# Kernel tuning notes

Hardware: AMD Instinct MI355X
Metric: run time of the kernel (lower is better)

## Reference

```python
import jax, jax.numpy as jnp
import numpy as np

B, S, HID = 2, 2048, 2048
NH, NKV, HD = 16, 4, 128
EPS = 1e-6
THETA = 10000.0
NEG = jnp.float32(-1e30)


def setup_inputs() -> dict:
    key = jax.random.key(0)
    ks = jax.random.split(key, 7)
    return {
        "hidden_states": jax.random.normal(ks[0], (B, S, HID), jnp.float32) * 0.02,
        "positions": jnp.broadcast_to(jnp.arange(S, dtype=jnp.int32), (B, S)),
        "Wq": jax.random.normal(ks[1], (HID, NH * HD), jnp.float32) * (HID ** -0.5),
        "Wk": jax.random.normal(ks[2], (HID, NKV * HD), jnp.float32) * (HID ** -0.5),
        "Wv": jax.random.normal(ks[3], (HID, NKV * HD), jnp.float32) * (HID ** -0.5),
        "Wc": jax.random.normal(ks[4], (NH * HD, HID), jnp.float32) * ((NH * HD) ** -0.5),
        "q_scale": jax.random.uniform(ks[5], (HD,), jnp.float32),
        "k_scale": jax.random.uniform(ks[6], (HD,), jnp.float32),
    }


def _rmsnorm(x, scale):
    # per-head RMSNorm over head_dim (nnx.RMSNorm semantics)
    return x * jax.lax.rsqrt(jnp.mean(x * x, axis=-1, keepdims=True) + EPS) * scale


def _rope_neox(x, positions):
    # x: [B, S, H, HD]; full rotary_dim == HD, neox style (split halves)
    half = HD // 2
    inv_freq = 1.0 / (THETA ** (jnp.arange(half, dtype=jnp.float32) / half))
    ang = positions[..., None].astype(jnp.float32) * inv_freq  # [B, S, half]
    cos = jnp.cos(ang)[:, :, None, :]
    sin = jnp.sin(ang)[:, :, None, :]
    x1, x2 = jnp.split(x, 2, axis=-1)
    return jnp.concatenate([x1 * cos - x2 * sin, x2 * cos + x1 * sin], axis=-1)


def reference(hidden_states, positions, Wq, Wk, Wv, Wc, q_scale, k_scale):
    q = (hidden_states @ Wq).reshape(B, S, NH, HD)
    k = (hidden_states @ Wk).reshape(B, S, NKV, HD)
    v = (hidden_states @ Wv).reshape(B, S, NKV, HD)
    q = _rmsnorm(q, q_scale)
    k = _rmsnorm(k, k_scale)
    q = _rope_neox(q, positions)
    k = _rope_neox(k, positions)
    # GQA: expand KV heads to query heads
    rep = NH // NKV
    k = jnp.repeat(k, rep, axis=2)
    v = jnp.repeat(v, rep, axis=2)
    scores = jnp.einsum("bqhd,bkhd->bhqk", q, k) * (HD ** -0.5)
    causal = jnp.tril(jnp.ones((S, S), dtype=bool))
    scores = jnp.where(causal, scores, NEG)
    probs = jax.nn.softmax(scores, axis=-1)
    attn = jnp.einsum("bhqk,bkhd->bqhd", probs, v).reshape(B, S, NH * HD)
    return attn @ Wc
```

## Files before the change

kernel.cpp:

```cpp
#include <hip/hip_runtime.h>
#include <stdint.h>

typedef unsigned short u16;
typedef unsigned int u32;
typedef __bf16 bf16x8 __attribute__((ext_vector_type(8)));
typedef float f32x4 __attribute__((ext_vector_type(4)));
typedef u32 u32x4 __attribute__((ext_vector_type(4)));

__device__ __forceinline__ u16 f2bf(float x){
  u32 u = __float_as_uint(x);
  u += 0x7FFFu + ((u >> 16) & 1u);
  return (u16)(u >> 16);
}
__device__ __forceinline__ float bf2f(u16 h){
  return __uint_as_float(((u32)h) << 16);
}
__device__ __forceinline__ u32 cvt_pk_bf16(float lo, float hi){
  u32 r;
  asm("v_cvt_pk_bf16_f32 %0, %1, %2" : "=v"(r) : "v"(lo), "v"(hi));
  return r;
}
__device__ __forceinline__ f32x4 mfma16(bf16x8 a, bf16x8 b, f32x4 c){
  return __builtin_amdgcn_mfma_f32_16x16x32_bf16(a, b, c, 0, 0, 0);
}
__device__ __forceinline__ void gload16(const void* g, const void* l){
  __builtin_amdgcn_global_load_lds(
      (__attribute__((address_space(1))) void*)(uintptr_t)g,
      (__attribute__((address_space(3))) void*)(u32)(uintptr_t)l,
      16, 0, 0);
}

__global__ void k_rope_table(float* __restrict__ ct, float* __restrict__ st){
  int idx = blockIdx.x * 256 + threadIdx.x;
  int p = idx >> 6, i = idx & 63;
  float freq = powf(10000.0f, -(float)i / 64.0f);
  float ang = (float)p * freq;
  ct[idx] = cosf(ang);
  st[idx] = sinf(ang);
}

__global__ void k_cast_bf16(const float* __restrict__ in, u16* __restrict__ out){
  int i = (blockIdx.x * 256 + threadIdx.x) * 4;
  float4 v = *(const float4*)(in + i);
  ushort4 o;
  o.x = f2bf(v.x); o.y = f2bf(v.y); o.z = f2bf(v.z); o.w = f2bf(v.w);
  *(ushort4*)(out + i) = o;
}

__global__ void k_trans_qkv(const float* __restrict__ Wq, const float* __restrict__ Wk,
                            const float* __restrict__ Wv, u16* __restrict__ out){
  __shared__ float tile[32][33];
  int nb = blockIdx.x * 32, kb = blockIdx.y * 32;
  int tx = threadIdx.x, ty = threadIdx.y;
  #pragma unroll
  for (int j = 0; j < 4; j++){
    int k = kb + ty + j*8;
    int n = nb + tx;
    float v;
    if (n < 2048)      v = Wq[(size_t)k*2048 + n];
    else if (n < 2560) v = Wk[(size_t)k*512 + (n - 2048)];
    else               v = Wv[(size_t)k*512 + (n - 2560)];
    tile[tx][ty + j*8] = v;
  }
  __syncthreads();
  #pragma unroll
  for (int j = 0; j < 4; j++){
    int n = nb + ty + j*8;
    out[(size_t)n*2048 + kb + tx] = f2bf(tile[ty + j*8][tx]);
  }
}

__global__ void k_trans_wc(const float* __restrict__ Wc, u16* __restrict__ out){
  __shared__ float tile[32][33];
  int nb = blockIdx.x * 32, kb = blockIdx.y * 32;
  int tx = threadIdx.x, ty = threadIdx.y;
  #pragma unroll
  for (int j = 0; j < 4; j++){
    tile[tx][ty + j*8] = Wc[(size_t)(kb + ty + j*8)*2048 + nb + tx];
  }
  __syncthreads();
  #pragma unroll
  for (int j = 0; j < 4; j++){
    out[(size_t)(nb + ty + j*8)*2048 + kb + tx] = f2bf(tile[ty + j*8][tx]);
  }
}

template<bool OBF>
__global__ __launch_bounds__(256) void k_gemm(const u16* __restrict__ A, const u16* __restrict__ Bt,
                                              void* __restrict__ Cv, int M, int N, int K, int nbx){
  __shared__ u16 As[2][128*32], Bs[2][128*32];
  int tid = threadIdx.x;
  int lane = tid & 63, w = tid >> 6;
  int g = lane >> 4, c16 = lane & 15;
  int wr = w >> 1, wc = w & 1;
  int chunk = gridDim.x >> 3;
  int logical = (blockIdx.x & 7) * chunk + (blockIdx.x >> 3);
  int bx = logical % nbx, by = logical / nbx;
  size_t bm = (size_t)by * 128, bn = (size_t)bx * 128;
  f32x4 zero = {0.f, 0.f, 0.f, 0.f};
  f32x4 acc[4][4];
  #pragma unroll
  for (int i=0;i<4;i++)
    #pragma unroll
    for (int j=0;j<4;j++) acc[i][j] = zero;

  int jj = (w*2)*64 + lane;
  int nt = K >> 5;
  #pragma unroll
  for (int p = 0; p < 2; p++){
    int j = jj + p*64;
    int r = j >> 2, slot = j & 3;
    gload16(A  + (bm + r)*(size_t)K + slot*8, (const char*)As[0] + (w*2+p)*1024);
    gload16(Bt + (bn + r)*(size_t)K + slot*8, (const char*)Bs[0] + (w*2+p)*1024);
  }
  asm volatile("s_waitcnt vmcnt(0)" ::: "memory");
  __builtin_amdgcn_s_barrier();

  int cur = 0;
  for (int t = 0; t < nt; ++t){
    if (t + 1 < nt){
      int k0 = (t + 1) << 5;
      #pragma unroll
      for (int p = 0; p < 2; p++){
        int j = jj + p*64;
        int r = j >> 2, slot = j & 3;
        gload16(A  + (bm + r)*(size_t)K + k0 + slot*8, (const char*)As[cur^1] + (w*2+p)*1024);
        gload16(Bt + (bn + r)*(size_t)K + k0 + slot*8, (const char*)Bs[cur^1] + (w*2+p)*1024);
      }
    }
    const u16* Ac = As[cur];
    const u16* Bc = Bs[cur];
    bf16x8 af[4], bfr[4];
    #pragma unroll
    for (int mi=0;mi<4;mi++) af[mi]  = *(const bf16x8*)&Ac[(wr*64 + mi*16 + c16)*32 + g*8];
    #pragma unroll
    for (int ni=0;ni<4;ni++) bfr[ni] = *(const bf16x8*)&Bc[(wc*64 + ni*16 + c16)*32 + g*8];
    #pragma unroll
    for (int mi=0;mi<4;mi++)
      #pragma unroll
      for (int ni=0;ni<4;ni++)
        acc[mi][ni] = mfma16(af[mi], bfr[ni], acc[mi][ni]);
    if (t + 1 < nt){
      asm volatile("s_waitcnt vmcnt(0)" ::: "memory");
      __builtin_amdgcn_s_barrier();
    }
    cur ^= 1;
  }
  #pragma unroll
  for (int mi=0;mi<4;mi++){
    #pragma unroll
    for (int ni=0;ni<4;ni++){
      #pragma unroll
      for (int r=0;r<4;r++){
        size_t row = bm + wr*64 + mi*16 + g*4 + r;
        size_t col = bn + wc*64 + ni*16 + c16;
        if (OBF) ((u16*)Cv)[row * (size_t)N + col] = f2bf(acc[mi][ni][r]);
        else     ((float*)Cv)[row * (size_t)N + col] = acc[mi][ni][r];
      }
    }
  }
}

__global__ __launch_bounds__(256) void k_norm_rope(const u16* __restrict__ qkv, const int* __restrict__ pos,
    const float* __restrict__ qsc, const float* __restrict__ ksc,
    const float* __restrict__ ct, const float* __restrict__ st,
    u16* __restrict__ qo, u16* __restrict__ ko){
  int bs = blockIdx.x;
  int hh = blockIdx.y * 4 + (threadIdx.x >> 6);
  int d = threadIdx.x & 63;
  int b = bs >> 11, s = bs & 2047;
  const u16* row = qkv + (size_t)bs * 3072 + hh * 128;
  u16 r1 = row[d], r2 = row[d + 64];
  float x1 = bf2f(r1), x2 = bf2f(r2);
  float ssq = x1*x1 + x2*x2;
  #pragma unroll
  for (int mm = 1; mm < 64; mm <<= 1) ssq += __shfl_xor(ssq, mm);
  float inv = rsqrtf(ssq * (1.0f/128.0f) + 1e-6f);
  const float* sc = (hh < 16) ? qsc : ksc;
  float y1 = x1 * inv * sc[d];
  float y2 = x2 * inv * sc[d + 64];
  int p = pos[bs];
  float c = ct[p*64 + d], sn = st[p*64 + d];
  float o1 = y1*c - y2*sn;
  float o2 = y2*c + y1*sn;
  if (hh < 16){
    o1 *= 0.08838834764831845f;
    o2 *= 0.08838834764831845f;
    size_t o = ((size_t)(b*16 + hh) * 2048 + s) * 128 + d;
    qo[o] = f2bf(o1); qo[o + 64] = f2bf(o2);
  } else {
    size_t o = ((size_t)(b*4 + (hh-16)) * 2048 + s) * 128 + d;
    ko[o] = f2bf(o1); ko[o + 64] = f2bf(o2);
  }
}

__global__ __launch_bounds__(256) void k_vtrans(const u16* __restrict__ qkv, u16* __restrict__ vt){
  __shared__ u16 tile[64][132];
  int s0 = blockIdx.x * 64, kvh = blockIdx.y, b = blockIdx.z;
  int t = threadIdx.x;
  int r = t >> 2, qd = (t & 3) * 32;
  const u16* src = qkv + ((size_t)(b*2048 + s0 + r)) * 3072 + 2560 + kvh*128 + qd;
  #pragma unroll
  for (int i = 0; i < 4; i++)
    *(uint4*)&tile[r][qd + i*8] = *(const uint4*)(src + i*8);
  __syncthreads();
  int d = t >> 1, c = (t & 1) * 32;
  u16* dst = vt + ((size_t)(b*4 + kvh) * 128 + d) * 2048 + s0 + c;
  #pragma unroll
  for (int i = 0; i < 4; i++){
    u16 tmp[8];
    #pragma unroll
    for (int j = 0; j < 8; j++) tmp[j] = tile[c + i*8 + j][d];
    *(uint4*)(dst + i*8) = *(const uint4*)tmp;
  }
}

__device__ __forceinline__ void stage_kv(int w, int lane, u16* ksb, u16* vsb,
                                         const u16* kp, const u16* vp, int c0){
  #pragma unroll
  for (int p = 0; p < 4; p++){
    int j = (w*4 + p)*64 + lane;
    int r = j >> 4, slot = j & 15;
    const u16* src = kp + (size_t)(c0 + r)*128 + ((slot ^ (r & 7)) << 3);
    gload16(src, (const char*)ksb + (w*4 + p)*1024);
  }
  #pragma unroll
  for (int p = 0; p < 4; p++){
    int j = (w*4 + p)*64 + lane;
    int r = j >> 3, slot = j & 7;
    const u16* src = vp + (size_t)r*2048 + c0 + ((slot ^ (r & 7)) << 3);
    gload16(src, (const char*)vsb + (w*4 + p)*1024);
  }
}

__device__ __forceinline__ void proc_group(f32x4 (&sacc)[4], float &m, float &l,
    f32x4 (&o)[8], int qrow, bool diag, int c0, int lane, int g, int c16,
    const u16* vsb){
  if (diag){
    #pragma unroll
    for (int nt = 0; nt < 4; nt++)
      #pragma unroll
      for (int r = 0; r < 4; r++)
        if (c0 + nt*16 + g*4 + r > qrow) sacc[nt][r] = -1e30f;
  }
  float mx = fmaxf(fmaxf(sacc[0][0], sacc[0][1]), fmaxf(sacc[0][2], sacc[0][3]));
  #pragma unroll
  for (int nt = 1; nt < 4; nt++)
    mx = fmaxf(mx, fmaxf(fmaxf(sacc[nt][0], sacc[nt][1]), fmaxf(sacc[nt][2], sacc[nt][3])));
  mx = fmaxf(mx, __shfl_xor(mx, 16));
  mx = fmaxf(mx, __shfl_xor(mx, 32));
  if (__any(mx > m + 8.f)){
    float mn = fmaxf(m, mx);
    float al = __expf(m - mn);
    m = mn; l *= al;
    float alr[4];
    #pragma unroll
    for (int r = 0; r < 4; r++) alr[r] = __shfl(al, (lane & 48) | (g*4 + r));
    #pragma unroll
    for (int dt = 0; dt < 8; dt++)
      #pragma unroll
      for (int r = 0; r < 4; r++) o[dt][r] *= alr[r];
  }
  float s = 0.f;
  #pragma unroll
  for (int nt = 0; nt < 4; nt++)
    #pragma unroll
    for (int r = 0; r < 4; r++){
      float p = __expf(sacc[nt][r] - m);
      sacc[nt][r] = p;
      s += p;
    }
  s += __shfl_xor(s, 16);
  s += __shfl_xor(s, 32);
  l += s;
  u32 pkA[4], pkB[4];
  #pragma unroll
  for (int a = 0; a < 4; a++){
    pkA[a] = cvt_pk_bf16(sacc[a][0], sacc[a][1]);
    pkB[a] = cvt_pk_bf16(sacc[a][2], sacc[a][3]);
  }
  int s0l = (((g*2    ) & 3) << 4) | c16;
  int s1l = (((g*2 + 1) & 3) << 4) | c16;
  bool hi = (g & 2) != 0;
  u32 v0A[4], v0B[4], v1A[4], v1B[4];
  #pragma unroll
  for (int a = 0; a < 4; a++){
    v0A[a] = (u32)__shfl((int)pkA[a], s0l);
    v0B[a] = (u32)__shfl((int)pkB[a], s0l);
    v1A[a] = (u32)__shfl((int)pkA[a], s1l);
    v1B[a] = (u32)__shfl((int)pkB[a], s1l);
  }
  __builtin_amdgcn_s_setprio(1);
  #pragma unroll
  for (int kk2 = 0; kk2 < 2; kk2++){
    u32x4 pw;
    pw.x = hi ? v0A[2*kk2+1] : v0A[2*kk2];
    pw.y = hi ? v0B[2*kk2+1] : v0B[2*kk2];
    pw.z = hi ? v1A[2*kk2+1] : v1A[2*kk2];
    pw.w = hi ? v1B[2*kk2+1] : v1B[2*kk2];
    bf16x8 pf = __builtin_bit_cast(bf16x8, pw);
    #pragma unroll
    for (int dt = 0; dt < 8; dt++){
      int d = dt*16 + c16;
      bf16x8 vf = *(const bf16x8*)&vsb[d*64 + (((kk2*4 + g) ^ (d & 7)) << 3)];
      o[dt] = mfma16(pf, vf, o[dt]);
    }
  }
  __builtin_amdgcn_s_setprio(0);
}

__global__ __launch_bounds__(256, 2) void k_attn(const u16* __restrict__ q, const u16* __restrict__ k,
    const u16* __restrict__ vt, u16* __restrict__ attn){
  __shared__ u16 Ks[2][64*128];
  __shared__ u16 Vs[2][128*64];
  int lane = threadIdx.x & 63, w = threadIdx.x >> 6;
  int g = lane >> 4, c16 = lane & 15;
  int bid = blockIdx.x;
  int logical = (bid & 7)*64 + (bid >> 3);
  int pi = logical & 15;
  int hb = logical >> 4;
  int h = hb & 15, b = hb >> 4;
  int kvh = h >> 2;
  int qbA = pi*64, qbB = (31 - pi)*64;
  int tmax = 31 - pi;
  const u16* qp = q  + ((size_t)(b*16 + h))  * 2048 * 128;
  const u16* kp = k  + ((size_t)(b*4 + kvh)) * 2048 * 128;
  const u16* vp = vt + ((size_t)(b*4 + kvh)) * 128 * 2048;

  int qrA = qbA + w*16 + c16, qrB = qbB + w*16 + c16;
  bf16x8 qfA[4], qfB[4];
  #pragma unroll
  for (int kk = 0; kk < 4; kk++){
    qfA[kk] = *(const bf16x8*)(qp + (size_t)qrA*128 + kk*32 + g*8);
    qfB[kk] = *(const bf16x8*)(qp + (size_t)qrB*128 + kk*32 + g*8);
  }
  asm volatile("s_waitcnt vmcnt(0)" ::: "memory");

  f32x4 zero = {0.f,0.f,0.f,0.f};
  f32x4 oA[8], oB[8];
  #pragma unroll
  for (int i=0;i<8;i++){ oA[i] = zero; oB[i] = zero; }
  float mA = -1e30f, mB = -1e30f, lA = 0.f, lB = 0.f;

  stage_kv(w, lane, Ks[0], Vs[0], kp, vp, 0);

  for (int t = 0; t <= tmax; t++){
    int c0 = t*64;
    if (t < tmax){
      stage_kv(w, lane, Ks[(t+1)&1], Vs[(t+1)&1], kp, vp, c0 + 64);
      asm volatile("s_waitcnt vmcnt(8)" ::: "memory");
    } else {
      asm volatile("s_waitcnt vmcnt(0)" ::: "memory");
    }
    __builtin_amdgcn_s_barrier();
    const u16* ksb = Ks[t&1];
    const u16* vsb = Vs[t&1];
    bool Aact = (t <= pi);
    f32x4 sA[4], sB[4];
    #pragma unroll
    for (int i=0;i<4;i++){ sA[i] = zero; sB[i] = zero; }
    __builtin_amdgcn_s_setprio(1);
    if (Aact){
      #pragma unroll
      for (int nt=0;nt<4;nt++){
        #pragma unroll
        for (int kk=0;kk<4;kk++){
          int row = nt*16 + c16;
          bf16x8 kf = *(const bf16x8*)&ksb[row*128 + (((kk*4 + g) ^ (row & 7)) << 3)];
          sB[nt] = mfma16(kf, qfB[kk], sB[nt]);
          sA[nt] = mfma16(kf, qfA[kk], sA[nt]);
        }
      }
    } else {
      #pragma unroll
      for (int nt=0;nt<4;nt++){
        #pragma unroll
        for (int kk=0;kk<4;kk++){
          int row = nt*16 + c16;
          bf16x8 kf = *(const bf16x8*)&ksb[row*128 + (((kk*4 + g) ^ (row & 7)) << 3)];
          sB[nt] = mfma16(kf, qfB[kk], sB[nt]);
        }
      }
    }
    __builtin_amdgcn_s_setprio(0);
    if (Aact) proc_group(sA, mA, lA, oA, qrA, t == pi, c0, lane, g, c16, vsb);
    proc_group(sB, mB, lB, oB, qrB, t == tmax, c0, lane, g, c16, vsb);
    __builtin_amdgcn_sched_barrier(0);
    asm volatile("s_waitcnt lgkmcnt(0)" ::: "memory");
    __builtin_amdgcn_s_barrier();
  }
  float lrA[4], lrB[4];
  #pragma unroll
  for (int r = 0; r < 4; r++){
    lrA[r] = __shfl(lA, (lane & 48) | (g*4 + r));
    lrB[r] = __shfl(lB, (lane & 48) | (g*4 + r));
  }
  #pragma unroll
  for (int dt=0;dt<8;dt++){
    #pragma unroll
    for (int r=0;r<4;r++){
      size_t orA = (size_t)b*2048 + qbA + w*16 + g*4 + r;
      size_t orB = (size_t)b*2048 + qbB + w*16 + g*4 + r;
      attn[orA*2048 + (size_t)h*128 + dt*16 + c16] = f2bf(oA[dt][r] / lrA[r]);
      attn[orB*2048 + (size_t)h*128 + dt*16 + c16] = f2bf(oB[dt][r] / lrB[r]);
    }
  }
}

extern "C" void kernel_launch(void* const* d_in, const int* in_sizes, int n_in,
                              void* d_out, int out_size, void* d_ws, size_t ws_size,
                              hipStream_t stream){
  const float* hidden    = (const float*)d_in[0];
  const int*   positions = (const int*)d_in[1];
  const float* Wq = (const float*)d_in[2];
  const float* Wk = (const float*)d_in[3];
  const float* Wv = (const float*)d_in[4];
  const float* Wc = (const float*)d_in[5];
  const float* qs = (const float*)d_in[6];
  const float* ks = (const float*)d_in[7];
  float* out = (float*)d_out;
  char* ws = (char*)d_ws;
  float* ct      = (float*)(ws + 0);
  float* st      = (float*)(ws + 524288);
  u16*   hid_bf  = (u16*)(ws + 1048576);
  u16*   attn_bf = hid_bf;
  u16*   wqkv_t  = (u16*)(ws + 17825792);
  u16*   wct     = (u16*)(ws + 30408704);
  u16*   qkv_bf  = (u16*)(ws + 38797312);
  u16*   q_bf    = (u16*)(ws + 63963136);
  u16*   k_bf    = (u16*)(ws + 80740352);
  u16*   vt_bf   = (u16*)(ws + 84934656);

  k_rope_table<<<512, 256, 0, stream>>>(ct, st);
  k_cast_bf16<<<8192, 256, 0, stream>>>(hidden, hid_bf);
  k_trans_qkv<<<dim3(96, 64), dim3(32, 8), 0, stream>>>(Wq, Wk, Wv, wqkv_t);
  k_trans_wc<<<dim3(64, 64), dim3(32, 8), 0, stream>>>(Wc, wct);
  k_gemm<true><<<768, 256, 0, stream>>>(hid_bf, wqkv_t, (void*)qkv_bf, 4096, 3072, 2048, 24);
  k_norm_rope<<<dim3(4096, 5), 256, 0, stream>>>(qkv_bf, positions, qs, ks, ct, st, q_bf, k_bf);
  k_vtrans<<<dim3(32, 4, 2), 256, 0, stream>>>(qkv_bf, vt_bf);
  k_attn<<<512, 256, 0, stream>>>(q_bf, k_bf, vt_bf, attn_bf);
  k_gemm<false><<<512, 256, 0, stream>>>(attn_bf, wct, (void*)out, 4096, 2048, 2048, 16);
}
```

Baseline: 222.2 us.

## Merge prep kernels into one launch and switch softmax to exp2 with log2e-folded scale

Merges the rope-table, hidden-cast and two weight-transpose kernels into a single block-indexed prep kernel, which removes three launches and the idle gaps between them. It also folds log2(e) into the query scale (0.0884*1.4427) so the attention softmax can use exp2f in place of __expf. The lazy-rescale threshold moves from 8 to 11.5 to keep the same bound in base-2 units. The merged kernel's branches differ in work per block, so some load imbalance is possible.

```diff
diff --git a/kernel.cpp b/kernel.cpp
--- a/kernel.cpp
+++ b/kernel.cpp
@@ -30,58 +30,66 @@
       16, 0, 0);
 }
 
-__global__ void k_rope_table(float* __restrict__ ct, float* __restrict__ st){
-  int idx = blockIdx.x * 256 + threadIdx.x;
-  int p = idx >> 6, i = idx & 63;
-  float freq = powf(10000.0f, -(float)i / 64.0f);
-  float ang = (float)p * freq;
-  ct[idx] = cosf(ang);
-  st[idx] = sinf(ang);
-}
-
-__global__ void k_cast_bf16(const float* __restrict__ in, u16* __restrict__ out){
-  int i = (blockIdx.x * 256 + threadIdx.x) * 4;
-  float4 v = *(const float4*)(in + i);
-  ushort4 o;
-  o.x = f2bf(v.x); o.y = f2bf(v.y); o.z = f2bf(v.z); o.w = f2bf(v.w);
-  *(ushort4*)(out + i) = o;
-}
-
-__global__ void k_trans_qkv(const float* __restrict__ Wq, const float* __restrict__ Wk,
-                            const float* __restrict__ Wv, u16* __restrict__ out){
+__global__ __launch_bounds__(256) void k_prep(const float* __restrict__ hidden,
+    const float* __restrict__ Wq, const float* __restrict__ Wk, const float* __restrict__ Wv,
+    const float* __restrict__ Wc, u16* __restrict__ hid_bf, u16* __restrict__ wqkv_t,
+    u16* __restrict__ wct, float* __restrict__ ct, float* __restrict__ st){
   __shared__ float tile[32][33];
-  int nb = blockIdx.x * 32, kb = blockIdx.y * 32;
-  int tx = threadIdx.x, ty = threadIdx.y;
-  #pragma unroll
-  for (int j = 0; j < 4; j++){
-    int k = kb + ty + j*8;
-    int n = nb + tx;
-    float v;
-    if (n < 2048)      v = Wq[(size_t)k*2048 + n];
-    else if (n < 2560) v = Wk[(size_t)k*512 + (n - 2048)];
-    else               v = Wv[(size_t)k*512 + (n - 2560)];
-    tile[tx][ty + j*8] = v;
-  }
-  __syncthreads();
-  #pragma unroll
-  for (int j = 0; j < 4; j++){
-    int n = nb + ty + j*8;
-    out[(size_t)n*2048 + kb + tx] = f2bf(tile[ty + j*8][tx]);
-  }
-}
-
-__global__ void k_trans_wc(const float* __restrict__ Wc, u16* __restrict__ out){
-  __shared__ float tile[32][33];
-  int nb = blockIdx.x * 32, kb = blockIdx.y * 32;
-  int tx = threadIdx.x, ty = threadIdx.y;
-  #pragma unroll
-  for (int j = 0; j < 4; j++){
-    tile[tx][ty + j*8] = Wc[(size_t)(kb + ty + j*8)*2048 + nb + tx];
-  }
-  __syncthreads();
-  #pragma unroll
-  for (int j = 0; j < 4; j++){
-    out[(size_t)(nb + ty + j*8)*2048 + kb + tx] = f2bf(tile[ty + j*8][tx]);
+  int bid = blockIdx.x;
+  int t = threadIdx.x;
+  if (bid < 8192){
+    int i = (bid * 256 + t) * 4;
+    float4 v = *(const float4*)(hidden + i);
+    ushort4 o;
+    o.x = f2bf(v.x); o.y = f2bf(v.y); o.z = f2bf(v.z); o.w = f2bf(v.w);
+    *(ushort4*)(hid_bf + i) = o;
+    return;
+  }
+  if (bid < 8192 + 6144){
+    int b2 = bid - 8192;
+    int nb = (b2 % 96) * 32, kb = (b2 / 96) * 32;
+    int tx = t & 31, ty = t >> 5;
+    #pragma unroll
+    for (int j = 0; j < 4; j++){
+      int k = kb + ty + j*8;
+      int n = nb + tx;
+      float v;
+      if (n < 2048)      v = Wq[(size_t)k*2048 + n];
+      else if (n < 2560) v = Wk[(size_t)k*512 + (n - 2048)];
+      else               v = Wv[(size_t)k*512 + (n - 2560)];
+      tile[tx][ty + j*8] = v;
+    }
+    __syncthreads();
+    #pragma unroll
+    for (int j = 0; j < 4; j++){
+      int n = nb + ty + j*8;
+      wqkv_t[(size_t)n*2048 + kb + tx] = f2bf(tile[ty + j*8][tx]);
+    }
+    return;
+  }
+  if (bid < 8192 + 6144 + 4096){
+    int b3 = bid - 8192 - 6144;
+    int nb = (b3 % 64) * 32, kb = (b3 / 64) * 32;
+    int tx = t & 31, ty = t >> 5;
+    #pragma unroll
+    for (int j = 0; j < 4; j++){
+      tile[tx][ty + j*8] = Wc[(size_t)(kb + ty + j*8)*2048 + nb + tx];
+    }
+    __syncthreads();
+    #pragma unroll
+    for (int j = 0; j < 4; j++){
+      wct[(size_t)(nb + ty + j*8)*2048 + kb + tx] = f2bf(tile[ty + j*8][tx]);
+    }
+    return;
+  }
+  {
+    int b4 = bid - 8192 - 6144 - 4096;
+    int idx = b4 * 256 + t;
+    int p = idx >> 6, i = idx & 63;
+    float freq = powf(10000.0f, -(float)i / 64.0f);
+    float ang = (float)p * freq;
+    ct[idx] = cosf(ang);
+    st[idx] = sinf(ang);
   }
 }
 
@@ -184,8 +192,8 @@
   float o1 = y1*c - y2*sn;
   float o2 = y2*c + y1*sn;
   if (hh < 16){
-    o1 *= 0.08838834764831845f;
-    o2 *= 0.08838834764831845f;
+    o1 *= 0.1275174528f;
+    o2 *= 0.1275174528f;
     size_t o = ((size_t)(b*16 + hh) * 2048 + s) * 128 + d;
     qo[o] = f2bf(o1); qo[o + 64] = f2bf(o2);
   } else {
@@ -249,9 +257,9 @@
     mx = fmaxf(mx, fmaxf(fmaxf(sacc[nt][0], sacc[nt][1]), fmaxf(sacc[nt][2], sacc[nt][3])));
   mx = fmaxf(mx, __shfl_xor(mx, 16));
   mx = fmaxf(mx, __shfl_xor(mx, 32));
-  if (__any(mx > m + 8.f)){
+  if (__any(mx > m + 11.5f)){
     float mn = fmaxf(m, mx);
-    float al = __expf(m - mn);
+    float al = exp2f(m - mn);
     m = mn; l *= al;
     float alr[4];
     #pragma unroll
@@ -266,7 +274,7 @@
   for (int nt = 0; nt < 4; nt++)
     #pragma unroll
     for (int r = 0; r < 4; r++){
-      float p = __expf(sacc[nt][r] - m);
+      float p = exp2f(sacc[nt][r] - m);
       sacc[nt][r] = p;
       s += p;
     }
@@ -431,10 +439,7 @@
   u16*   k_bf    = (u16*)(ws + 80740352);
   u16*   vt_bf   = (u16*)(ws + 84934656);
 
-  k_rope_table<<<512, 256, 0, stream>>>(ct, st);
-  k_cast_bf16<<<8192, 256, 0, stream>>>(hidden, hid_bf);
-  k_trans_qkv<<<dim3(96, 64), dim3(32, 8), 0, stream>>>(Wq, Wk, Wv, wqkv_t);
-  k_trans_wc<<<dim3(64, 64), dim3(32, 8), 0, stream>>>(Wc, wct);
+  k_prep<<<18944, 256, 0, stream>>>(hidden, Wq, Wk, Wv, Wc, hid_bf, wqkv_t, wct, ct, st);
   k_gemm<true><<<768, 256, 0, stream>>>(hid_bf, wqkv_t, (void*)qkv_bf, 4096, 3072, 2048, 24);
   k_norm_rope<<<dim3(4096, 5), 256, 0, stream>>>(qkv_bf, positions, qs, ks, ct, st, q_bf, k_bf);
   k_vtrans<<<dim3(32, 4, 2), 256, 0, stream>>>(qkv_bf, vt_bf);
```

Measured after the change: 216.1 us. 2.7% less time.
